# Optimization experiments

Measured on AMD Instinct MI355X. Metric: run time of the kernel, lower is better.

Reference implementation:

```python
import jax, jax.numpy as jnp
import numpy as np

H = 256

def setup_inputs() -> dict:
    key = jax.random.key(0)
    ks = jax.random.split(key, 9)
    s = 1.0 / np.sqrt(H)
    x = jax.random.normal(ks[0], (8, 2048, H), dtype=jnp.float32)
    Wq = jax.random.uniform(ks[1], (H, H), jnp.float32, -s, s)
    bq = jax.random.uniform(ks[2], (H,), jnp.float32, -s, s)
    Wk = jax.random.uniform(ks[3], (H, H), jnp.float32, -s, s)
    bk = jax.random.uniform(ks[4], (H,), jnp.float32, -s, s)
    Wv = jax.random.uniform(ks[5], (H, H), jnp.float32, -s, s)
    bv = jax.random.uniform(ks[6], (H,), jnp.float32, -s, s)
    Ww = jax.random.uniform(ks[7], (H, 1), jnp.float32, -s, s)
    bw = jax.random.uniform(ks[8], (1,), jnp.float32, -s, s)
    return {"x": x, "Wq": Wq, "bq": bq, "Wk": Wk, "bk": bk,
            "Wv": Wv, "bv": bv, "Ww": Ww, "bw": bw}

def reference(x, Wq, bq, Wk, bk, Wv, bv, Ww, bw):
    # x: (B, N, H) — cross-asset attention over N assets
    q = x @ Wq + bq
    k = x @ Wk + bk
    v = x @ Wv + bv
    scale = 1.0 / jnp.sqrt(jnp.asarray(q.shape[-1], q.dtype))
    beta = jnp.einsum('bnd,bmd->bnm', q, k) * scale  # (B, N, N)
    beta = jax.nn.softmax(beta, axis=-1)
    # original: sum(value[:,None] * beta[...,None], dim=2) == beta @ v
    out = jnp.einsum('bnm,bmd->bnd', beta, v)
    final_scores = (out @ Ww + bw)[..., 0]  # (B, N)
    return final_scores
```

## Files before the change

kernel.cpp:

```cpp
#include <hip/hip_runtime.h>

#define H 256
#define NB 2048
#define BATCH 8
#define NSPLIT 8
#define KSPAN (NB / NSPLIT)
#define NHALF (KSPAN / 32)

typedef unsigned short u16;
using bf16x8 = __attribute__((ext_vector_type(8))) __bf16;
using f32x4  = __attribute__((ext_vector_type(4))) float;

typedef const __attribute__((address_space(1))) void gv_t;
typedef __attribute__((address_space(3))) void lv_t;

__device__ __forceinline__ void gl_lds16(const void* g, void* l) {
    __builtin_amdgcn_global_load_lds((gv_t*)g, (lv_t*)l, 16, 0, 0);
}

#define MFMA(a, b, c) __builtin_amdgcn_mfma_f32_16x16x32_bf16(a, b, c, 0, 0, 0)

__device__ __forceinline__ u16 f2bf(float f) {
    union { float f; unsigned u; } v; v.f = f;
    unsigned r = v.u + 0x7fffu + ((v.u >> 16) & 1u);
    return (u16)(r >> 16);
}

__global__ __launch_bounds__(256) void wprep_kernel(
        const float* __restrict__ Wq, const float* __restrict__ Wk,
        const float* __restrict__ Wv, const float* __restrict__ Ww,
        const float* __restrict__ bq,
        u16* __restrict__ wqb, u16* __restrict__ wkb,
        float* __restrict__ wvw, float* __restrict__ kbv) {
    int f = blockIdx.x, t = threadIdx.x;
    float wq = Wq[f * H + t];
    wqb[f * H + t] = f2bf(wq);
    float wk = Wk[f * H + t];
    wkb[f * H + t] = f2bf(wk);
    float p = Wv[f * H + t] * Ww[t];
    float r = wk * bq[t];
    for (int o = 32; o; o >>= 1) { p += __shfl_xor(p, o); r += __shfl_xor(r, o); }
    __shared__ float redp[4], redr[4];
    int w = t >> 6, lane = t & 63;
    if (lane == 0) { redp[w] = p; redr[w] = r; }
    __syncthreads();
    if (t == 0) {
        wvw[f] = redp[0] + redp[1] + redp[2] + redp[3];
        kbv[f] = redr[0] + redr[1] + redr[2] + redr[3];
    }
}

__global__ __launch_bounds__(256) void cvtu_kernel(
        const float* __restrict__ x, const float* __restrict__ wvw,
        const float* __restrict__ kbv, const float* __restrict__ bv,
        const float* __restrict__ Ww,
        u16* __restrict__ xbf, float2* __restrict__ uee) {
    int lane = threadIdx.x & 63;
    int row  = blockIdx.x * 4 + (threadIdx.x >> 6);
    float4 xv = *(const float4*)(x + row * H + lane * 4);
    ushort4 o;
    o.x = f2bf(xv.x); o.y = f2bf(xv.y); o.z = f2bf(xv.z); o.w = f2bf(xv.w);
    *(ushort4*)(xbf + row * H + lane * 4) = o;
    float4 wv = *(const float4*)(wvw + lane * 4);
    float s = xv.x * wv.x + xv.y * wv.y + xv.z * wv.z + xv.w * wv.w;
    float4 kv = *(const float4*)(kbv + lane * 4);
    float d = xv.x * kv.x + xv.y * kv.y + xv.z * kv.z + xv.w * kv.w;
    float4 bvv = *(const float4*)(bv + lane * 4);
    float4 www = *(const float4*)(Ww + lane * 4);
    float c = bvv.x * www.x + bvv.y * www.y + bvv.z * www.z + bvv.w * www.w;
    for (int o2 = 32; o2; o2 >>= 1) {
        s += __shfl_xor(s, o2); d += __shfl_xor(d, o2); c += __shfl_xor(c, o2);
    }
    if (lane == 0) {
        float e = __expf(d * 0.0625f);
        uee[row] = make_float2(e * (s + c), e);
    }
}

__global__ __launch_bounds__(256) void gemm_bt_kernel(
        const u16* __restrict__ A, const u16* __restrict__ B,
        u16* __restrict__ C, float scale) {
    __shared__ u16 bt[16384];
    int tid = threadIdx.x;
    int mb = blockIdx.x * 128, nb = blockIdx.y * 64;
    int w = tid >> 6, lane = tid & 63;
    int l15 = lane & 15, quad = lane >> 4;

    {
        const u16* gsrc = B + (nb + w * 16 + l15) * H + quad * 8;
        for (int ks = 0; ks < 8; ++ks)
            gl_lds16(gsrc + ks * 32, bt + (w * 8 + ks) * 512);
    }

    bf16x8 a[2][8];
    for (int mi = 0; mi < 2; ++mi) {
        const u16* abase = A + (size_t)(mb + w * 32 + mi * 16 + l15) * H + quad * 8;
        for (int ks = 0; ks < 8; ++ks) a[mi][ks] = *(const bf16x8*)(abase + ks * 32);
    }
    __syncthreads();

    f32x4 acc[2][4] = {};
    for (int ks = 0; ks < 8; ++ks)
        for (int t = 0; t < 4; ++t) {
            bf16x8 b = *(const bf16x8*)(bt + ((t * 8 + ks) * 64 + lane) * 8);
            acc[0][t] = MFMA(a[0][ks], b, acc[0][t]);
            acc[1][t] = MFMA(a[1][ks], b, acc[1][t]);
        }

    for (int mi = 0; mi < 2; ++mi) {
        int m = mb + w * 32 + mi * 16 + quad * 4;
        for (int t = 0; t < 4; ++t) {
            int n = nb + t * 16 + l15;
            for (int r = 0; r < 4; ++r)
                C[(size_t)(m + r) * H + n] = f2bf(acc[mi][t][r] * scale);
        }
    }
}

__global__ __launch_bounds__(256, 4) void attn_kernel(
        const u16* __restrict__ T, const u16* __restrict__ xbf,
        const float2* __restrict__ uee,
        float* __restrict__ pnum, float* __restrict__ pden) {
    __shared__ u16 kt[16384];
    int tid = threadIdx.x;
    int b = blockIdx.y, qb = blockIdx.x * 128, sp = blockIdx.z;
    int w = tid >> 6, lane = tid & 63, l15 = lane & 15, quad = lane >> 4;

    bf16x8 aq[2][8];
    for (int mi = 0; mi < 2; ++mi) {
        const u16* qbase = T + (size_t)(b * NB + qb + w * 32 + mi * 16 + l15) * H + quad * 8;
        for (int ks = 0; ks < 8; ++ks) aq[mi][ks] = *(const bf16x8*)(qbase + ks * 32);
    }

    const u16* xb = xbf + (size_t)b * NB * H;
    const float2* uep = uee + (size_t)b * NB;
    const int kb0 = sp * KSPAN;

    int c0 = w * 4;
    {
        const u16* g = xb + (size_t)(kb0 + (c0 >> 3) * 16 + l15) * H + (c0 & 7) * 32 + quad * 8;
        for (int j = 0; j < 4; ++j) {
            int c = c0 + j;
            gl_lds16(xb + (size_t)(kb0 + (c >> 3) * 16 + l15) * H + (c & 7) * 32 + quad * 8,
                     kt + c * 512);
        }
        (void)g;
    }
    __syncthreads();

    float ls[2][4] = {}, as_[2][4] = {};

    #pragma unroll 1
    for (int h = 0; h < NHALF; ++h) {
        int cur = h & 1;
        if (h + 1 < NHALF) {
            int kb32 = kb0 + (h + 1) * 32;
            u16* dst = kt + (cur ^ 1) * 8192;
            for (int j = 0; j < 4; ++j) {
                int c = c0 + j;
                gl_lds16(xb + (size_t)(kb32 + (c >> 3) * 16 + l15) * H + (c & 7) * 32 + quad * 8,
                         dst + c * 512);
            }
        }
        int kb32 = kb0 + h * 32;
        float2 ue0 = uep[kb32 + l15];
        float2 ue1 = uep[kb32 + 16 + l15];

        const u16* ktc = kt + cur * 8192;
        f32x4 acc[2][2] = {};
        for (int ks = 0; ks < 8; ++ks)
            for (int t = 0; t < 2; ++t) {
                bf16x8 bfr = *(const bf16x8*)(ktc + ((t * 8 + ks) * 64 + lane) * 8);
                acc[0][t] = MFMA(aq[0][ks], bfr, acc[0][t]);
                acc[1][t] = MFMA(aq[1][ks], bfr, acc[1][t]);
            }

        for (int mi = 0; mi < 2; ++mi)
            for (int r = 0; r < 4; ++r) {
                float p0 = __expf(acc[mi][0][r]);
                float p1 = __expf(acc[mi][1][r]);
                as_[mi][r] += p0 * ue0.x + p1 * ue1.x;
                ls[mi][r]  += p0 * ue0.y + p1 * ue1.y;
            }
        __syncthreads();
    }

    for (int mi = 0; mi < 2; ++mi)
        for (int r = 0; r < 4; ++r)
            for (int o = 1; o < 16; o <<= 1) {
                ls[mi][r]  += __shfl_xor(ls[mi][r], o);
                as_[mi][r] += __shfl_xor(as_[mi][r], o);
            }

    if (l15 == 0) {
        for (int mi = 0; mi < 2; ++mi) {
            size_t base = (size_t)(sp * BATCH + b) * NB + qb + w * 32 + mi * 16 + quad * 4;
            for (int r = 0; r < 4; ++r) {
                pnum[base + r] = as_[mi][r];
                pden[base + r] = ls[mi][r];
            }
        }
    }
}

__global__ __launch_bounds__(256) void finalize_kernel(
        const float* __restrict__ pnum, const float* __restrict__ pden,
        const float* __restrict__ bw, float* __restrict__ out) {
    int i = blockIdx.x * 256 + threadIdx.x;
    float num = 0.f, den = 0.f;
    for (int sp = 0; sp < NSPLIT; ++sp) {
        num += pnum[sp * (BATCH * NB) + i];
        den += pden[sp * (BATCH * NB) + i];
    }
    out[i] = num / den + bw[0];
}

extern "C" void kernel_launch(void* const* d_in, const int* in_sizes, int n_in,
                              void* d_out, int out_size, void* d_ws, size_t ws_size,
                              hipStream_t stream) {
    (void)in_sizes; (void)n_in; (void)out_size; (void)ws_size;
    const float* x  = (const float*)d_in[0];
    const float* Wq = (const float*)d_in[1];
    const float* bq = (const float*)d_in[2];
    const float* Wk = (const float*)d_in[3];
    const float* bk = (const float*)d_in[4];  (void)bk;
    const float* Wv = (const float*)d_in[5];
    const float* bv = (const float*)d_in[6];
    const float* Ww = (const float*)d_in[7];
    const float* bw = (const float*)d_in[8];
    float* out = (float*)d_out;

    u16* xbf = (u16*)d_ws;
    u16* Tbf = xbf + 4194304;
    u16* aTb = Tbf + 4194304;
    u16* wqb = aTb + 65536;
    u16* wkb = wqb + 65536;
    float* wvw = (float*)(wkb + 65536);
    float* kbv = wvw + 256;
    float2* uee = (float2*)(kbv + 256);
    float* pnum = (float*)(uee + 16384);
    float* pden = pnum + NSPLIT * BATCH * NB;

    hipLaunchKernelGGL(wprep_kernel, dim3(256), dim3(256), 0, stream,
                       Wq, Wk, Wv, Ww, bq, wqb, wkb, wvw, kbv);
    hipLaunchKernelGGL(gemm_bt_kernel, dim3(2, 4), dim3(256), 0, stream,
                       wkb, wqb, aTb, 0.0625f);
    hipLaunchKernelGGL(cvtu_kernel, dim3(4096), dim3(256), 0, stream,
                       x, wvw, kbv, bv, Ww, xbf, uee);
    hipLaunchKernelGGL(gemm_bt_kernel, dim3(128, 4), dim3(256), 0, stream,
                       xbf, aTb, Tbf, 1.0f);
    hipLaunchKernelGGL(attn_kernel, dim3(16, 8, NSPLIT), dim3(256), 0, stream,
                       Tbf, xbf, uee, pnum, pden);
    hipLaunchKernelGGL(finalize_kernel, dim3(64), dim3(256), 0, stream,
                       pnum, pden, bw, out);
}
```

Measured before the change: 129.1 us.

## Drop LDS staging in attention kernel; single-wave blocks load K fragments directly

The attention kernel now runs one 64-thread wave per block, with a flat grid whose block index puts batch in the low bits. Each wave loads its key fragments straight from global memory into registers, double-buffered 16 keys at a time, and the loop is fully unrolled. This removes the shared-memory staging and the __syncthreads barriers. In exchange, every wave fetches its own copy of the keys instead of sharing them across four waves, which relies on L2 reuse and raises register pressure.

```diff
diff --git a/kernel.cpp b/kernel.cpp
--- a/kernel.cpp
+++ b/kernel.cpp
@@ -5,7 +5,7 @@
 #define BATCH 8
 #define NSPLIT 8
 #define KSPAN (NB / NSPLIT)
-#define NHALF (KSPAN / 32)
+#define NCHUNK (KSPAN / 16)
 
 typedef unsigned short u16;
 using bf16x8 = __attribute__((ext_vector_type(8))) __bf16;
@@ -117,75 +117,70 @@
     }
 }
 
-__global__ __launch_bounds__(256, 4) void attn_kernel(
+__global__ __launch_bounds__(64, 3) void attn_kernel(
         const u16* __restrict__ T, const u16* __restrict__ xbf,
         const float2* __restrict__ uee,
         float* __restrict__ pnum, float* __restrict__ pden) {
-    __shared__ u16 kt[16384];
-    int tid = threadIdx.x;
-    int b = blockIdx.y, qb = blockIdx.x * 128, sp = blockIdx.z;
-    int w = tid >> 6, lane = tid & 63, l15 = lane & 15, quad = lane >> 4;
+    int id = blockIdx.x;
+    int b = id & 7, rest = id >> 3;
+    int qc = rest & 63, sp = rest >> 6;
+    int lane = threadIdx.x;
+    int l15 = lane & 15, quad = lane >> 4;
 
     bf16x8 aq[2][8];
-    for (int mi = 0; mi < 2; ++mi) {
-        const u16* qbase = T + (size_t)(b * NB + qb + w * 32 + mi * 16 + l15) * H + quad * 8;
-        for (int ks = 0; ks < 8; ++ks) aq[mi][ks] = *(const bf16x8*)(qbase + ks * 32);
-    }
-
-    const u16* xb = xbf + (size_t)b * NB * H;
-    const float2* uep = uee + (size_t)b * NB;
-    const int kb0 = sp * KSPAN;
-
-    int c0 = w * 4;
     {
-        const u16* g = xb + (size_t)(kb0 + (c0 >> 3) * 16 + l15) * H + (c0 & 7) * 32 + quad * 8;
-        for (int j = 0; j < 4; ++j) {
-            int c = c0 + j;
-            gl_lds16(xb + (size_t)(kb0 + (c >> 3) * 16 + l15) * H + (c & 7) * 32 + quad * 8,
-                     kt + c * 512);
-        }
-        (void)g;
-    }
-    __syncthreads();
+        const u16* qbase = T + (size_t)(b * NB + qc * 32 + l15) * H + quad * 8;
+        #pragma unroll
+        for (int mi = 0; mi < 2; ++mi)
+            #pragma unroll
+            for (int ks = 0; ks < 8; ++ks)
+                aq[mi][ks] = *(const bf16x8*)(qbase + mi * 16 * H + ks * 32);
+    }
+
+    const u16* xb = xbf + ((size_t)b * NB + sp * KSPAN) * H;
+    const float2* uep = uee + (size_t)b * NB + sp * KSPAN;
+
+    bf16x8 bfr[2][8];
+    float2 uv[2];
+    {
+        const u16* krow = xb + (size_t)l15 * H + quad * 8;
+        #pragma unroll
+        for (int ks = 0; ks < 8; ++ks) bfr[0][ks] = *(const bf16x8*)(krow + ks * 32);
+        uv[0] = uep[l15];
+    }
 
     float ls[2][4] = {}, as_[2][4] = {};
 
-    #pragma unroll 1
-    for (int h = 0; h < NHALF; ++h) {
-        int cur = h & 1;
-        if (h + 1 < NHALF) {
-            int kb32 = kb0 + (h + 1) * 32;
-            u16* dst = kt + (cur ^ 1) * 8192;
-            for (int j = 0; j < 4; ++j) {
-                int c = c0 + j;
-                gl_lds16(xb + (size_t)(kb32 + (c >> 3) * 16 + l15) * H + (c & 7) * 32 + quad * 8,
-                         dst + c * 512);
+    #pragma unroll
+    for (int ch = 0; ch < NCHUNK; ++ch) {
+        int cur = ch & 1;
+        if (ch + 1 < NCHUNK) {
+            const u16* nrow = xb + (size_t)((ch + 1) * 16 + l15) * H + quad * 8;
+            #pragma unroll
+            for (int ks = 0; ks < 8; ++ks)
+                bfr[cur ^ 1][ks] = *(const bf16x8*)(nrow + ks * 32);
+            uv[cur ^ 1] = uep[(ch + 1) * 16 + l15];
+        }
+        f32x4 acc[2] = {};
+        #pragma unroll
+        for (int ks = 0; ks < 8; ++ks) {
+            acc[0] = MFMA(aq[0][ks], bfr[cur][ks], acc[0]);
+            acc[1] = MFMA(aq[1][ks], bfr[cur][ks], acc[1]);
+        }
+        float uex = uv[cur].x, uey = uv[cur].y;
+        #pragma unroll
+        for (int mi = 0; mi < 2; ++mi)
+            #pragma unroll
+            for (int r = 0; r < 4; ++r) {
+                float p = __expf(acc[mi][r]);
+                as_[mi][r] += p * uex;
+                ls[mi][r]  += p * uey;
             }
-        }
-        int kb32 = kb0 + h * 32;
-        float2 ue0 = uep[kb32 + l15];
-        float2 ue1 = uep[kb32 + 16 + l15];
-
-        const u16* ktc = kt + cur * 8192;
-        f32x4 acc[2][2] = {};
-        for (int ks = 0; ks < 8; ++ks)
-            for (int t = 0; t < 2; ++t) {
-                bf16x8 bfr = *(const bf16x8*)(ktc + ((t * 8 + ks) * 64 + lane) * 8);
-                acc[0][t] = MFMA(aq[0][ks], bfr, acc[0][t]);
-                acc[1][t] = MFMA(aq[1][ks], bfr, acc[1][t]);
-            }
-
-        for (int mi = 0; mi < 2; ++mi)
-            for (int r = 0; r < 4; ++r) {
-                float p0 = __expf(acc[mi][0][r]);
-                float p1 = __expf(acc[mi][1][r]);
-                as_[mi][r] += p0 * ue0.x + p1 * ue1.x;
-                ls[mi][r]  += p0 * ue0.y + p1 * ue1.y;
-            }
-        __syncthreads();
-    }
-
+    }
+
+    #pragma unroll
     for (int mi = 0; mi < 2; ++mi)
+        #pragma unroll
         for (int r = 0; r < 4; ++r)
             for (int o = 1; o < 16; o <<= 1) {
                 ls[mi][r]  += __shfl_xor(ls[mi][r], o);
@@ -193,13 +188,14 @@
             }
 
     if (l15 == 0) {
-        for (int mi = 0; mi < 2; ++mi) {
-            size_t base = (size_t)(sp * BATCH + b) * NB + qb + w * 32 + mi * 16 + quad * 4;
+        size_t base = (size_t)(sp * BATCH + b) * NB + qc * 32 + quad * 4;
+        #pragma unroll
+        for (int mi = 0; mi < 2; ++mi)
+            #pragma unroll
             for (int r = 0; r < 4; ++r) {
-                pnum[base + r] = as_[mi][r];
-                pden[base + r] = ls[mi][r];
+                pnum[base + mi * 16 + r] = as_[mi][r];
+                pden[base + mi * 16 + r] = ls[mi][r];
             }
-        }
     }
 }
 
@@ -249,7 +245,7 @@
                        x, wvw, kbv, bv, Ww, xbf, uee);
     hipLaunchKernelGGL(gemm_bt_kernel, dim3(128, 4), dim3(256), 0, stream,
                        xbf, aTb, Tbf, 1.0f);
-    hipLaunchKernelGGL(attn_kernel, dim3(16, 8, NSPLIT), dim3(256), 0, stream,
+    hipLaunchKernelGGL(attn_kernel, dim3(64 * BATCH * NSPLIT), dim3(64), 0, stream,
                        Tbf, xbf, uee, pnum, pden);
     hipLaunchKernelGGL(finalize_kernel, dim3(64), dim3(256), 0, stream,
                        pnum, pden, bw, out);
```

Result: slower. 204.0 us (+58.1%).

## Double query rows per attention block to reuse each staged key tile

Applied to the files above, without the earlier changes.

Each attention block now covers 256 query rows instead of 128, with four 16-row MFMA tiles per wave. Every key tile loaded into LDS is therefore reused across twice as many queries, which halves global/LDS key traffic and barrier count per unit of work. The grid is flattened to 1D with batch in the low bits, and the occupancy hint drops from 4 to 2 blocks because the query fragments and accumulators need more registers. The grid also halves to 512 blocks, which lowers parallelism on a machine with many CUs.

```diff
diff --git a/kernel.cpp b/kernel.cpp
--- a/kernel.cpp
+++ b/kernel.cpp
@@ -117,45 +117,50 @@
     }
 }
 
-__global__ __launch_bounds__(256, 4) void attn_kernel(
+__global__ __launch_bounds__(256, 2) void attn_kernel(
         const u16* __restrict__ T, const u16* __restrict__ xbf,
         const float2* __restrict__ uee,
         float* __restrict__ pnum, float* __restrict__ pden) {
     __shared__ u16 kt[16384];
     int tid = threadIdx.x;
-    int b = blockIdx.y, qb = blockIdx.x * 128, sp = blockIdx.z;
+    int id = blockIdx.x;
+    int b = id & 7, rest = id >> 3;
+    int qc = rest & 7, sp = rest >> 3;
     int w = tid >> 6, lane = tid & 63, l15 = lane & 15, quad = lane >> 4;
-
-    bf16x8 aq[2][8];
-    for (int mi = 0; mi < 2; ++mi) {
-        const u16* qbase = T + (size_t)(b * NB + qb + w * 32 + mi * 16 + l15) * H + quad * 8;
-        for (int ks = 0; ks < 8; ++ks) aq[mi][ks] = *(const bf16x8*)(qbase + ks * 32);
+    int qb = qc * 256;
+
+    bf16x8 aq[4][8];
+    {
+        const u16* qbase = T + (size_t)(b * NB + qb + w * 64 + l15) * H + quad * 8;
+        #pragma unroll
+        for (int mi = 0; mi < 4; ++mi)
+            #pragma unroll
+            for (int ks = 0; ks < 8; ++ks)
+                aq[mi][ks] = *(const bf16x8*)(qbase + mi * 16 * H + ks * 32);
     }
 
     const u16* xb = xbf + (size_t)b * NB * H;
     const float2* uep = uee + (size_t)b * NB;
     const int kb0 = sp * KSPAN;
-
     int c0 = w * 4;
-    {
-        const u16* g = xb + (size_t)(kb0 + (c0 >> 3) * 16 + l15) * H + (c0 & 7) * 32 + quad * 8;
-        for (int j = 0; j < 4; ++j) {
-            int c = c0 + j;
-            gl_lds16(xb + (size_t)(kb0 + (c >> 3) * 16 + l15) * H + (c & 7) * 32 + quad * 8,
-                     kt + c * 512);
-        }
-        (void)g;
+
+    #pragma unroll
+    for (int j = 0; j < 4; ++j) {
+        int c = c0 + j;
+        gl_lds16(xb + (size_t)(kb0 + (c >> 3) * 16 + l15) * H + (c & 7) * 32 + quad * 8,
+                 kt + c * 512);
     }
     __syncthreads();
 
-    float ls[2][4] = {}, as_[2][4] = {};
+    float ls[4][4] = {}, as_[4][4] = {};
 
     #pragma unroll 1
     for (int h = 0; h < NHALF; ++h) {
-        int cur = h & 1;
+        const u16* ktc = kt + (h & 1) * 8192;
         if (h + 1 < NHALF) {
             int kb32 = kb0 + (h + 1) * 32;
-            u16* dst = kt + (cur ^ 1) * 8192;
+            u16* dst = kt + ((h & 1) ^ 1) * 8192;
+            #pragma unroll
             for (int j = 0; j < 4; ++j) {
                 int c = c0 + j;
                 gl_lds16(xb + (size_t)(kb32 + (c >> 3) * 16 + l15) * H + (c & 7) * 32 + quad * 8,
@@ -163,29 +168,36 @@
             }
         }
         int kb32 = kb0 + h * 32;
-        float2 ue0 = uep[kb32 + l15];
-        float2 ue1 = uep[kb32 + 16 + l15];
-
-        const u16* ktc = kt + cur * 8192;
-        f32x4 acc[2][2] = {};
+        float2 uv0 = uep[kb32 + l15];
+        float2 uv1 = uep[kb32 + 16 + l15];
+
+        f32x4 acc[4][2] = {};
+        #pragma unroll
         for (int ks = 0; ks < 8; ++ks)
+            #pragma unroll
             for (int t = 0; t < 2; ++t) {
                 bf16x8 bfr = *(const bf16x8*)(ktc + ((t * 8 + ks) * 64 + lane) * 8);
                 acc[0][t] = MFMA(aq[0][ks], bfr, acc[0][t]);
                 acc[1][t] = MFMA(aq[1][ks], bfr, acc[1][t]);
-            }
-
-        for (int mi = 0; mi < 2; ++mi)
+                acc[2][t] = MFMA(aq[2][ks], bfr, acc[2][t]);
+                acc[3][t] = MFMA(aq[3][ks], bfr, acc[3][t]);
+            }
+
+        #pragma unroll
+        for (int mi = 0; mi < 4; ++mi)
+            #pragma unroll
             for (int r = 0; r < 4; ++r) {
                 float p0 = __expf(acc[mi][0][r]);
                 float p1 = __expf(acc[mi][1][r]);
-                as_[mi][r] += p0 * ue0.x + p1 * ue1.x;
-                ls[mi][r]  += p0 * ue0.y + p1 * ue1.y;
+                as_[mi][r] += p0 * uv0.x + p1 * uv1.x;
+                ls[mi][r]  += p0 * uv0.y + p1 * uv1.y;
             }
         __syncthreads();
     }
 
-    for (int mi = 0; mi < 2; ++mi)
+    #pragma unroll
+    for (int mi = 0; mi < 4; ++mi)
+        #pragma unroll
         for (int r = 0; r < 4; ++r)
             for (int o = 1; o < 16; o <<= 1) {
                 ls[mi][r]  += __shfl_xor(ls[mi][r], o);
@@ -193,13 +205,14 @@
             }
 
     if (l15 == 0) {
-        for (int mi = 0; mi < 2; ++mi) {
-            size_t base = (size_t)(sp * BATCH + b) * NB + qb + w * 32 + mi * 16 + quad * 4;
+        size_t base = (size_t)(sp * BATCH + b) * NB + qb + w * 64 + quad * 4;
+        #pragma unroll
+        for (int mi = 0; mi < 4; ++mi)
+            #pragma unroll
             for (int r = 0; r < 4; ++r) {
-                pnum[base + r] = as_[mi][r];
-                pden[base + r] = ls[mi][r];
-            }
-        }
+                pnum[base + mi * 16 + r] = as_[mi][r];
+                pden[base + mi * 16 + r] = ls[mi][r];
+            }
     }
 }
 
@@ -249,7 +262,7 @@
                        x, wvw, kbv, bv, Ww, xbf, uee);
     hipLaunchKernelGGL(gemm_bt_kernel, dim3(128, 4), dim3(256), 0, stream,
                        xbf, aTb, Tbf, 1.0f);
-    hipLaunchKernelGGL(attn_kernel, dim3(16, 8, NSPLIT), dim3(256), 0, stream,
+    hipLaunchKernelGGL(attn_kernel, dim3(8 * 8 * NSPLIT), dim3(256), 0, stream,
                        Tbf, xbf, uee, pnum, pden);
     hipLaunchKernelGGL(finalize_kernel, dim3(64), dim3(256), 0, stream,
                        pnum, pden, bw, out);
```

After: 126.4 us. 2.0% less time.
